# Kernel optimization log

Measured on AMD Instinct MI355X. Metric: run time of the kernel, lower is better.

## Reference

```python
import jax, jax.numpy as jnp
import numpy as np

SAMPLE_NUMS = 9
VIEW_RANGE = 2      # args.max_turn_view_range
TEMP = 0.07         # args.temperature
AVG_EPS = 1e-6      # BertAVG eps
COS_EPS = 1e-8      # torch.cosine_similarity eps


def setup_inputs() -> dict:
    key = jax.random.key(0)
    k0, k1, k2 = jax.random.split(key, 3)
    G, S, H = 8, 512, 768            # groups, max_seq_length, hidden_size
    B = G * SAMPLE_NUMS              # 72 flattened dialogues
    self_output = jax.random.normal(k0, (B, S, H), dtype=jnp.float32)
    attention_mask = jnp.ones((B, S), dtype=jnp.float32)
    qa_ids = jax.random.randint(k1, (B, S), 0, 4, dtype=jnp.int32)
    turn_ids = jnp.sort(jax.random.randint(k2, (B, S), 0, 16, dtype=jnp.int32), axis=-1)
    labels = jnp.zeros((G, SAMPLE_NUMS), dtype=jnp.float32).at[:, 0].set(1.0)
    return {"self_output": self_output, "attention_mask": attention_mask,
            "labels": labels, "qa_ids": qa_ids, "turn_ids": turn_ids}


def _masked_avg(x, m):
    # BertAVG: sum over seq of x*m / (sum(m) + eps)   x:[B,S,H] m:[B,S]
    return jnp.sum(x * m[..., None], axis=1) / (jnp.sum(m, axis=1, keepdims=True) + AVG_EPS)


def _cos(x, y):
    # torch.cosine_similarity over last dim, eps-clamped norms
    dot = jnp.sum(x * y, axis=-1)
    nx = jnp.maximum(jnp.linalg.norm(x, axis=-1), COS_EPS)
    ny = jnp.maximum(jnp.linalg.norm(y, axis=-1), COS_EPS)
    c = dot / (nx * ny)
    c = jnp.where(c == 1.0, jnp.nan, c)   # cos[cos==1] = nan
    return c / TEMP


def _calc_loss(pred, labels):
    return -jnp.nanmean(jax.nn.log_softmax(pred, axis=-1) * labels)


def reference(self_output, attention_mask, labels, qa_ids, turn_ids):
    H = self_output.shape[-1]
    # role masks from qa_ids
    q_mask = ((qa_ids == 1) | (qa_ids == 2)).astype(self_output.dtype)
    a_mask = ((qa_ids == 0) | (qa_ids == 2)).astype(self_output.dtype)
    n_mask = (qa_ids == 3).astype(self_output.dtype)
    q_am = attention_mask * q_mask
    a_am = attention_mask * a_mask
    n_am = attention_mask * n_mask
    q_so = self_output * q_am[..., None]   # [B,S,H]
    a_so = self_output * a_am[..., None]
    n_so = self_output * n_am[..., None]
    # role-masked cross scores [B,S,S]
    q_w = jnp.einsum('bsh,bth->bst', q_so, a_so + n_so)
    a_w = jnp.einsum('bsh,bth->bst', a_so, q_so + n_so)
    n_w = jnp.einsum('bsh,bth->bst', n_so, q_so + a_so)
    # turn-range band mask: |turn_s - turn_t| <= range
    dt = turn_ids[:, :, None] - turn_ids[:, None, :]
    band = (jnp.abs(dt) <= VIEW_RANGE).astype(self_output.dtype)  # [B,S,S]
    filtered_w = (q_w + a_w + n_w) * band
    # cross outputs
    q_co = jnp.einsum('bst,bth->bsh', filtered_w, q_so)
    a_co = jnp.einsum('bst,bth->bsh', filtered_w, a_so)
    n_co = jnp.einsum('bst,bth->bsh', filtered_w, n_so)
    # masked averages
    q_self = _masked_avg(q_so, q_am)
    q_cross = _masked_avg(q_co, a_am + n_am)
    a_self = _masked_avg(a_so, a_am)
    a_cross = _masked_avg(a_co, q_am + n_am)
    n_self = _masked_avg(n_so, n_am)
    n_cross = _masked_avg(n_co, q_am + a_am)
    # [G, sample_nums, H]
    q_self = q_self.reshape(-1, SAMPLE_NUMS, H)
    q_cross = q_cross.reshape(-1, SAMPLE_NUMS, H)
    a_self = a_self.reshape(-1, SAMPLE_NUMS, H)
    a_cross = a_cross.reshape(-1, SAMPLE_NUMS, H)
    n_self = n_self.reshape(-1, SAMPLE_NUMS, H)
    n_cross = n_cross.reshape(-1, SAMPLE_NUMS, H)
    q_output = q_self[:, 0, :]
    a_output = a_self[:, 0, :]
    n_output = n_self[:, 0, :]
    # vectorized over sample axis (replaces the python loop + stack)
    logit_q = _cos(q_self, q_cross)  # [G, sample_nums]
    logit_a = _cos(a_self, a_cross)
    logit_n = _cos(n_self, n_cross)
    stage_loss = (_calc_loss(logit_a, labels) + _calc_loss(logit_q, labels)
                  + _calc_loss(logit_n, labels)) / 3.0
    return (stage_loss, q_output, a_output, n_output)
```

## Files before the change

kernel.cpp:

```cpp
#include <hip/hip_runtime.h>
#include <math.h>

#define BB 72
#define SS 512
#define HH 768
#define GG 8
#define SN 9
#define VR 2
#define NT 16
#define NPART 16


__device__ float g_W[(size_t)BB * NT * 4 * HH];
__device__ float g_snum[BB * 3 * HH];
__device__ float g_xpart[(size_t)BB * NPART * 3 * HH];
__device__ float g_logits[3 * BB];

__device__ __forceinline__ void class_masks(float am, int id, float& qv, float& av, float& nv) {
    qv = (id == 1 || id == 2) ? am : 0.0f;
    av = (id == 0 || id == 2) ? am : 0.0f;
    nv = (id == 3) ? am : 0.0f;
}

__global__ void k_g(const float* __restrict__ x, const float* __restrict__ am,
                    const int* __restrict__ qa, const int* __restrict__ turn) {
    __shared__ float Gs[NT * 4 * 4 * 64];
    __shared__ int   tn[SS];
    __shared__ float c2[SS];
    __shared__ int   idv[SS];

    const int b = blockIdx.y, hbase = blockIdx.x * 256;
    const int tid = threadIdx.x, w = tid >> 6, lane = tid & 63;

    for (int i = tid; i < SS; i += 512) {
        tn[i] = turn[b * SS + i];
        float a = am[b * SS + i]; c2[i] = a * a;
        idv[i] = qa[b * SS + i];
    }
    {
        const float4 z = make_float4(0.f, 0.f, 0.f, 0.f);
        for (int i = tid * 4; i < NT * 4 * 4 * 64; i += 2048) *(float4*)&Gs[i] = z;
    }
    __syncthreads();

    const int s0 = w * 64;
    const float* xbase = x + ((size_t)b * SS + s0) * HH + hbase + lane * 4;
    float r[4][4];
#pragma unroll
    for (int i = 0; i < 4; ++i)
#pragma unroll
        for (int k = 0; k < 4; ++k) r[i][k] = 0.0f;
    int cur = tn[s0];

    float4 A[4], Bq[4];
#define LDQ(buf, c) { _Pragma("unroll") for (int j_ = 0; j_ < 4; ++j_)          \
        buf[j_] = *(const float4*)(xbase + (size_t)((c) * 4 + j_) * HH); }
#define FLUSH() { _Pragma("unroll") for (int i_ = 0; i_ < 4; ++i_) {            \
        _Pragma("unroll") for (int k_ = 0; k_ < 4; ++k_) {                      \
            atomicAdd(&Gs[((cur * 4 + i_) * 4 + k_) * 64 + lane], r[i_][k_]);   \
            r[i_][k_] = 0.0f; } } }
#define CONSUME(buf, c) { _Pragma("unroll") for (int j_ = 0; j_ < 4; ++j_) {    \
        const int s_ = s0 + (c) * 4 + j_;                                       \
        const int v_ = tn[s_];                                                  \
        if (v_ != cur) { FLUSH(); cur = v_; }                                   \
        const float c2_ = c2[s_];                                               \
        const int id_ = idv[s_];                                                \
        const float4 xv_ = buf[j_];                                             \
        if (id_ == 0) { r[0][0] += xv_.x * c2_; r[0][1] += xv_.y * c2_;         \
                        r[0][2] += xv_.z * c2_; r[0][3] += xv_.w * c2_; }       \
        else if (id_ == 1) { r[1][0] += xv_.x * c2_; r[1][1] += xv_.y * c2_;    \
                             r[1][2] += xv_.z * c2_; r[1][3] += xv_.w * c2_; }  \
        else if (id_ == 2) { r[2][0] += xv_.x * c2_; r[2][1] += xv_.y * c2_;    \
                             r[2][2] += xv_.z * c2_; r[2][3] += xv_.w * c2_; }  \
        else { r[3][0] += xv_.x * c2_; r[3][1] += xv_.y * c2_;                  \
               r[3][2] += xv_.z * c2_; r[3][3] += xv_.w * c2_; } } }

    LDQ(A, 0);
    for (int c = 0; c < 16; c += 2) {
        LDQ(Bq, c + 1);
        CONSUME(A, c);
        if (c + 2 < 16) LDQ(A, c + 2);
        CONSUME(Bq, c + 1);
    }
    FLUSH();
#undef LDQ
#undef FLUSH
#undef CONSUME
    __syncthreads();

#pragma unroll
    for (int vv = 0; vv < 2; ++vv) {
        const int v = w * 2 + vv;
        const int ulo = (v - VR < 0) ? 0 : v - VR;
        const int uhi = (v + VR > NT - 1) ? NT - 1 : v + VR;
        float acc[4][4];
#pragma unroll
        for (int i = 0; i < 4; ++i)
#pragma unroll
            for (int k = 0; k < 4; ++k) acc[i][k] = 0.0f;
        for (int u = ulo; u <= uhi; ++u) {
#pragma unroll
            for (int i = 0; i < 4; ++i)
#pragma unroll
                for (int k = 0; k < 4; ++k)
                    acc[i][k] += Gs[((u * 4 + i) * 4 + k) * 64 + lane];
        }
        float* Wo = g_W + ((size_t)(b * NT + v) * 4) * HH + hbase + lane * 4;
#pragma unroll
        for (int i = 0; i < 4; ++i) {
            float4 o; o.x = acc[i][0]; o.y = acc[i][1]; o.z = acc[i][2]; o.w = acc[i][3];
            *(float4*)(Wo + (size_t)i * HH) = o;
        }
    }
    if (w == 0) {
        float t[4][4];
#pragma unroll
        for (int i = 0; i < 4; ++i)
#pragma unroll
            for (int k = 0; k < 4; ++k) t[i][k] = 0.0f;
        for (int u = 0; u < NT; ++u) {
#pragma unroll
            for (int i = 0; i < 4; ++i)
#pragma unroll
                for (int k = 0; k < 4; ++k)
                    t[i][k] += Gs[((u * 4 + i) * 4 + k) * 64 + lane];
        }
        float4 oq, oa, on;
        oq.x = t[1][0] + t[2][0]; oq.y = t[1][1] + t[2][1];
        oq.z = t[1][2] + t[2][2]; oq.w = t[1][3] + t[2][3];
        oa.x = t[0][0] + t[2][0]; oa.y = t[0][1] + t[2][1];
        oa.z = t[0][2] + t[2][2]; oa.w = t[0][3] + t[2][3];
        on.x = t[3][0]; on.y = t[3][1]; on.z = t[3][2]; on.w = t[3][3];
        *(float4*)(g_snum + (size_t)(b * 3 + 0) * HH + hbase + lane * 4) = oq;
        *(float4*)(g_snum + (size_t)(b * 3 + 1) * HH + hbase + lane * 4) = oa;
        *(float4*)(g_snum + (size_t)(b * 3 + 2) * HH + hbase + lane * 4) = on;
    }
}

__global__ __launch_bounds__(256) void k_ct(const float* __restrict__ x,
                                            const float* __restrict__ am,
                                            const int* __restrict__ qa,
                                            const int* __restrict__ turn) {
    __shared__ float red[4][3 * HH];
    __shared__ int   tnb[32];
    __shared__ float amb[32];
    __shared__ int   idb[32];

    const int b = blockIdx.y, ts = blockIdx.x, T0 = ts * 32;
    const int tid = threadIdx.x, w = tid >> 6, lane = tid & 63;
    if (tid < 32) {
        tnb[tid] = turn[b * SS + T0 + tid];
        amb[tid] = am[b * SS + T0 + tid];
        idb[tid] = qa[b * SS + T0 + tid];
    }
    __syncthreads();

    const float* xb = x + (size_t)b * SS * HH;
    float4 xt[8][3];
#pragma unroll
    for (int it = 0; it < 8; ++it) {
        const float* xr = xb + (size_t)(T0 + w * 8 + it) * HH + lane * 4;
        xt[it][0] = *(const float4*)(xr + 0);
        xt[it][1] = *(const float4*)(xr + 256);
        xt[it][2] = *(const float4*)(xr + 512);
    }

    float xn[3][12];
#pragma unroll
    for (int c = 0; c < 3; ++c)
#pragma unroll
        for (int k = 0; k < 12; ++k) xn[c][k] = 0.0f;

    float4 Wr[4][3];
    int curv = -1;

#pragma unroll
    for (int it = 0; it < 8; ++it) {
        const int tl = w * 8 + it;
        const int v = tnb[tl];
        if (v != curv) {
            curv = v;
            const float* Wg = g_W + ((size_t)(b * NT + v) * 4) * HH + lane * 4;
#pragma unroll
            for (int i = 0; i < 4; ++i) {
                Wr[i][0] = *(const float4*)(Wg + (size_t)i * HH + 0);
                Wr[i][1] = *(const float4*)(Wg + (size_t)i * HH + 256);
                Wr[i][2] = *(const float4*)(Wg + (size_t)i * HH + 512);
            }
        }
        float d[4];
#pragma unroll
        for (int i = 0; i < 4; ++i) {
            float s = 0;
#pragma unroll
            for (int ch = 0; ch < 3; ++ch) {
                s += xt[it][ch].x * Wr[i][ch].x + xt[it][ch].y * Wr[i][ch].y
                   + xt[it][ch].z * Wr[i][ch].z + xt[it][ch].w * Wr[i][ch].w;
            }
            d[i] = s;
        }
#pragma unroll
        for (int off = 32; off; off >>= 1) {
#pragma unroll
            for (int i = 0; i < 4; ++i) d[i] += __shfl_xor(d[i], off);
        }
        float qt, at, nt; class_masks(amb[tl], idb[tl], qt, at, nt);
        const float ant = at + nt, qnt = qt + nt, qat = qt + at;
        const float Sqq = d[1] + d[2], Sqa = d[2], Saa = d[0] + d[2], Snn = d[3];
        const float cwq = qt * (ant * Sqa + qnt * Saa + qat * Snn);
        const float cwa = at * (ant * Sqq + qnt * Sqa + qat * Snn);
        const float cwn = nt * (ant * (Sqq + Sqa) + qnt * (Sqa + Saa));
#pragma unroll
        for (int ch = 0; ch < 3; ++ch) {
            const float4 xv = xt[it][ch];
            xn[0][ch * 4 + 0] += cwq * xv.x; xn[0][ch * 4 + 1] += cwq * xv.y;
            xn[0][ch * 4 + 2] += cwq * xv.z; xn[0][ch * 4 + 3] += cwq * xv.w;
            xn[1][ch * 4 + 0] += cwa * xv.x; xn[1][ch * 4 + 1] += cwa * xv.y;
            xn[1][ch * 4 + 2] += cwa * xv.z; xn[1][ch * 4 + 3] += cwa * xv.w;
            xn[2][ch * 4 + 0] += cwn * xv.x; xn[2][ch * 4 + 1] += cwn * xv.y;
            xn[2][ch * 4 + 2] += cwn * xv.z; xn[2][ch * 4 + 3] += cwn * xv.w;
        }
    }

#pragma unroll
    for (int c = 0; c < 3; ++c) {
#pragma unroll
        for (int ch = 0; ch < 3; ++ch) {
            float4 o;
            o.x = xn[c][ch * 4 + 0]; o.y = xn[c][ch * 4 + 1];
            o.z = xn[c][ch * 4 + 2]; o.w = xn[c][ch * 4 + 3];
            *(float4*)&red[w][c * HH + ch * 256 + lane * 4] = o;
        }
    }
    __syncthreads();
    float* xo = g_xpart + (size_t)(b * NPART + ts) * 3 * HH;
    for (int idx = tid * 4; idx < 3 * HH; idx += 1024) {
        float4 r0 = *(float4*)&red[0][idx];
        float4 r1 = *(float4*)&red[1][idx];
        float4 r2 = *(float4*)&red[2][idx];
        float4 r3 = *(float4*)&red[3][idx];
        float4 o;
        o.x = r0.x + r1.x + r2.x + r3.x;
        o.y = r0.y + r1.y + r2.y + r3.y;
        o.z = r0.z + r1.z + r2.z + r3.z;
        o.w = r0.w + r1.w + r2.w + r3.w;
        *(float4*)(xo + idx) = o;
    }
}

__global__ void k_cos(const float* __restrict__ am, const int* __restrict__ qa,
                      float* __restrict__ out) {
    const int c = blockIdx.x, b = blockIdx.y, tid = threadIdx.x;
    const int wave = tid >> 6, lane = tid & 63;
    __shared__ float redd[4][3];
    __shared__ float sD[3];

    float q = 0, a = 0, n = 0;
    for (int s = tid; s < SS; s += 256) {
        float m = am[b * SS + s]; int id = qa[b * SS + s];
        float qv, av, nv; class_masks(m, id, qv, av, nv);
        q += qv; a += av; n += nv;
    }
#pragma unroll
    for (int off = 32; off; off >>= 1) {
        q += __shfl_down(q, off); a += __shfl_down(a, off); n += __shfl_down(n, off);
    }
    if (lane == 0) { redd[wave][0] = q; redd[wave][1] = a; redd[wave][2] = n; }
    __syncthreads();
    if (tid == 0) {
        float Q = 0, A = 0, N = 0;
#pragma unroll
        for (int w = 0; w < 4; ++w) { Q += redd[w][0]; A += redd[w][1]; N += redd[w][2]; }
        sD[0] = Q; sD[1] = A; sD[2] = N;
    }
    __syncthreads();
    const float Dq = sD[0], Da = sD[1], Dn = sD[2];
    const float Dself = (c == 0) ? Dq : ((c == 1) ? Da : Dn);
    const float Dcross = (c == 0) ? (Da + Dn) : ((c == 1) ? (Dq + Dn) : (Dq + Da));
    const float invS = 1.0f / (Dself + 1e-6f), invC = 1.0f / (Dcross + 1e-6f);

    float dot = 0, n1 = 0, n2 = 0;
#pragma unroll
    for (int j = 0; j < 3; ++j) {
        const int h = tid + j * 256;
        float sv = g_snum[(size_t)(b * 3 + c) * HH + h];
        float cv = 0;
        const float* xp = g_xpart + ((size_t)b * NPART * 3 + c) * HH + h;
#pragma unroll
        for (int p = 0; p < NPART; ++p) cv += xp[(size_t)p * 3 * HH];
        sv *= invS; cv *= invC;
        dot += sv * cv; n1 += sv * sv; n2 += cv * cv;
        if (b % SN == 0)
            out[1 + ((size_t)c * GG + b / SN) * HH + h] = sv;
    }
#pragma unroll
    for (int off = 32; off; off >>= 1) {
        dot += __shfl_down(dot, off); n1 += __shfl_down(n1, off); n2 += __shfl_down(n2, off);
    }
    __shared__ float red2[4][3];
    if (lane == 0) { red2[wave][0] = dot; red2[wave][1] = n1; red2[wave][2] = n2; }
    __syncthreads();
    if (tid == 0) {
        float D = 0, N1 = 0, N2 = 0;
#pragma unroll
        for (int w = 0; w < 4; ++w) { D += red2[w][0]; N1 += red2[w][1]; N2 += red2[w][2]; }
        float nx = fmaxf(sqrtf(N1), 1e-8f);
        float ny = fmaxf(sqrtf(N2), 1e-8f);
        float cc = D / (nx * ny);
        if (cc == 1.0f) cc = __uint_as_float(0x7FC00000u);
        g_logits[c * BB + b] = cc / 0.07f;
    }
}

__global__ void k_loss(const float* __restrict__ labels, float* __restrict__ out) {
    __shared__ float rs[24];
    __shared__ int rc[24];
    const int tid = threadIdx.x;
    if (tid < 24) {
        int c = tid / GG, g = tid % GG;
        float lg[SN]; bool anynan = false;
        for (int j = 0; j < SN; ++j) {
            float v = g_logits[c * BB + g * SN + j];
            lg[j] = v;
            anynan = anynan || isnan(v);
        }
        float ssum = 0; int cnt = 0;
        if (!anynan) {
            float m = -1e30f;
            for (int j = 0; j < SN; ++j) m = fmaxf(m, lg[j]);
            float se = 0;
            for (int j = 0; j < SN; ++j) se += expf(lg[j] - m);
            float lse = m + logf(se);
            for (int j = 0; j < SN; ++j) ssum += (lg[j] - lse) * labels[g * SN + j];
            cnt = SN;
        }
        rs[tid] = ssum; rc[tid] = cnt;
    }
    __syncthreads();
    if (tid == 0) {
        float total = 0;
        for (int c = 0; c < 3; ++c) {
            float s = 0; int n = 0;
            for (int g = 0; g < GG; ++g) { s += rs[c * GG + g]; n += rc[c * GG + g]; }
            total += -(s / (float)n);
        }
        out[0] = total / 3.0f;
    }
}

extern "C" void kernel_launch(void* const* d_in, const int* in_sizes, int n_in,
                              void* d_out, int out_size, void* d_ws, size_t ws_size,
                              hipStream_t stream) {
    const float* x      = (const float*)d_in[0];
    const float* am     = (const float*)d_in[1];
    const float* labels = (const float*)d_in[2];
    const int*   qa     = (const int*)d_in[3];
    const int*   turn   = (const int*)d_in[4];
    float* out = (float*)d_out;

    k_g   <<<dim3(HH / 256, BB), 512, 0, stream>>>(x, am, qa, turn);
    k_ct  <<<dim3(SS / 32, BB),  256, 0, stream>>>(x, am, qa, turn);
    k_cos <<<dim3(3, BB),        256, 0, stream>>>(am, qa, out);
    k_loss<<<dim3(1),            64,  0, stream>>>(labels, out);
}
```

Baseline: 241.6 us.

## Split per-turn accumulation across sequence chunks with global atomics, defer window sums

The per-turn class accumulation kernel now runs over 8 sequence chunks per (batch, hidden slice), giving many more blocks. Partial results go to a zeroed global buffer through global atomics instead of shared-memory atomics. The view-range window sum moves into k_ct, and the full-sequence self sums move into k_cos, which now read the raw per-turn table. This trades extra global atomics, a zeroing kernel, and repeated window-sum reads for more parallelism in the first stage.

```diff
diff --git a/kernel.cpp b/kernel.cpp
--- a/kernel.cpp
+++ b/kernel.cpp
@@ -11,8 +11,7 @@
 #define NPART 16
 
 
-__device__ float g_W[(size_t)BB * NT * 4 * HH];
-__device__ float g_snum[BB * 3 * HH];
+__device__ float g_G[(size_t)BB * NT * 4 * HH];
 __device__ float g_xpart[(size_t)BB * NPART * 3 * HH];
 __device__ float g_logits[3 * BB];
 
@@ -22,119 +21,71 @@
     nv = (id == 3) ? am : 0.0f;
 }
 
-__global__ void k_g(const float* __restrict__ x, const float* __restrict__ am,
-                    const int* __restrict__ qa, const int* __restrict__ turn) {
-    __shared__ float Gs[NT * 4 * 4 * 64];
-    __shared__ int   tn[SS];
-    __shared__ float c2[SS];
-    __shared__ int   idv[SS];
-
-    const int b = blockIdx.y, hbase = blockIdx.x * 256;
+__global__ void k_zero() {
+    const size_t i = ((size_t)blockIdx.x * 256 + threadIdx.x) * 4;
+    *(float4*)&g_G[i] = make_float4(0.f, 0.f, 0.f, 0.f);
+}
+
+__global__ __launch_bounds__(256) void k_g(const float* __restrict__ x,
+                                           const float* __restrict__ am,
+                                           const int* __restrict__ qa,
+                                           const int* __restrict__ turn) {
+    __shared__ int   tn[64];
+    __shared__ float c2[64];
+    __shared__ int   idv[64];
+
+    const int b = blockIdx.y, hbase = blockIdx.x * 256, s0b = blockIdx.z * 64;
     const int tid = threadIdx.x, w = tid >> 6, lane = tid & 63;
 
-    for (int i = tid; i < SS; i += 512) {
-        tn[i] = turn[b * SS + i];
-        float a = am[b * SS + i]; c2[i] = a * a;
-        idv[i] = qa[b * SS + i];
-    }
-    {
-        const float4 z = make_float4(0.f, 0.f, 0.f, 0.f);
-        for (int i = tid * 4; i < NT * 4 * 4 * 64; i += 2048) *(float4*)&Gs[i] = z;
-    }
-    __syncthreads();
-
-    const int s0 = w * 64;
-    const float* xbase = x + ((size_t)b * SS + s0) * HH + hbase + lane * 4;
+    if (tid < 64) {
+        const int s = s0b + tid;
+        tn[tid] = turn[b * SS + s];
+        float a = am[b * SS + s]; c2[tid] = a * a;
+        idv[tid] = qa[b * SS + s];
+    }
+    __syncthreads();
+
+    const int sw = w * 16;
+    const float* xbase = x + ((size_t)(b * SS + s0b + sw)) * HH + hbase + lane * 4;
+
+    float4 xr[16];
+#pragma unroll
+    for (int j = 0; j < 16; ++j)
+        xr[j] = *(const float4*)(xbase + (size_t)j * HH);
+
     float r[4][4];
 #pragma unroll
     for (int i = 0; i < 4; ++i)
 #pragma unroll
         for (int k = 0; k < 4; ++k) r[i][k] = 0.0f;
-    int cur = tn[s0];
-
-    float4 A[4], Bq[4];
-#define LDQ(buf, c) { _Pragma("unroll") for (int j_ = 0; j_ < 4; ++j_)          \
-        buf[j_] = *(const float4*)(xbase + (size_t)((c) * 4 + j_) * HH); }
-#define FLUSH() { _Pragma("unroll") for (int i_ = 0; i_ < 4; ++i_) {            \
-        _Pragma("unroll") for (int k_ = 0; k_ < 4; ++k_) {                      \
-            atomicAdd(&Gs[((cur * 4 + i_) * 4 + k_) * 64 + lane], r[i_][k_]);   \
-            r[i_][k_] = 0.0f; } } }
-#define CONSUME(buf, c) { _Pragma("unroll") for (int j_ = 0; j_ < 4; ++j_) {    \
-        const int s_ = s0 + (c) * 4 + j_;                                       \
-        const int v_ = tn[s_];                                                  \
-        if (v_ != cur) { FLUSH(); cur = v_; }                                   \
-        const float c2_ = c2[s_];                                               \
-        const int id_ = idv[s_];                                                \
-        const float4 xv_ = buf[j_];                                             \
-        if (id_ == 0) { r[0][0] += xv_.x * c2_; r[0][1] += xv_.y * c2_;         \
-                        r[0][2] += xv_.z * c2_; r[0][3] += xv_.w * c2_; }       \
-        else if (id_ == 1) { r[1][0] += xv_.x * c2_; r[1][1] += xv_.y * c2_;    \
-                             r[1][2] += xv_.z * c2_; r[1][3] += xv_.w * c2_; }  \
-        else if (id_ == 2) { r[2][0] += xv_.x * c2_; r[2][1] += xv_.y * c2_;    \
-                             r[2][2] += xv_.z * c2_; r[2][3] += xv_.w * c2_; }  \
-        else { r[3][0] += xv_.x * c2_; r[3][1] += xv_.y * c2_;                  \
-               r[3][2] += xv_.z * c2_; r[3][3] += xv_.w * c2_; } } }
-
-    LDQ(A, 0);
-    for (int c = 0; c < 16; c += 2) {
-        LDQ(Bq, c + 1);
-        CONSUME(A, c);
-        if (c + 2 < 16) LDQ(A, c + 2);
-        CONSUME(Bq, c + 1);
+    int cur = tn[sw];
+
+#define FLUSH() {                                                              \
+    float* gb_ = g_G + ((size_t)(b * NT + cur) * 4) * HH + hbase + lane * 4;   \
+    _Pragma("unroll") for (int i_ = 0; i_ < 4; ++i_)                           \
+        _Pragma("unroll") for (int k_ = 0; k_ < 4; ++k_) {                     \
+            atomicAdd(gb_ + (size_t)i_ * HH + k_, r[i_][k_]);                  \
+            r[i_][k_] = 0.0f; } }
+
+#pragma unroll
+    for (int j = 0; j < 16; ++j) {
+        const int sl = sw + j;
+        const int v = tn[sl];
+        if (v != cur) { FLUSH(); cur = v; }
+        const float cc = c2[sl];
+        const int id = idv[sl];
+        const float4 xv = xr[j];
+        if (id == 0) { r[0][0] += xv.x * cc; r[0][1] += xv.y * cc;
+                       r[0][2] += xv.z * cc; r[0][3] += xv.w * cc; }
+        else if (id == 1) { r[1][0] += xv.x * cc; r[1][1] += xv.y * cc;
+                            r[1][2] += xv.z * cc; r[1][3] += xv.w * cc; }
+        else if (id == 2) { r[2][0] += xv.x * cc; r[2][1] += xv.y * cc;
+                            r[2][2] += xv.z * cc; r[2][3] += xv.w * cc; }
+        else { r[3][0] += xv.x * cc; r[3][1] += xv.y * cc;
+               r[3][2] += xv.z * cc; r[3][3] += xv.w * cc; }
     }
     FLUSH();
-#undef LDQ
 #undef FLUSH
-#undef CONSUME
-    __syncthreads();
-
-#pragma unroll
-    for (int vv = 0; vv < 2; ++vv) {
-        const int v = w * 2 + vv;
-        const int ulo = (v - VR < 0) ? 0 : v - VR;
-        const int uhi = (v + VR > NT - 1) ? NT - 1 : v + VR;
-        float acc[4][4];
-#pragma unroll
-        for (int i = 0; i < 4; ++i)
-#pragma unroll
-            for (int k = 0; k < 4; ++k) acc[i][k] = 0.0f;
-        for (int u = ulo; u <= uhi; ++u) {
-#pragma unroll
-            for (int i = 0; i < 4; ++i)
-#pragma unroll
-                for (int k = 0; k < 4; ++k)
-                    acc[i][k] += Gs[((u * 4 + i) * 4 + k) * 64 + lane];
-        }
-        float* Wo = g_W + ((size_t)(b * NT + v) * 4) * HH + hbase + lane * 4;
-#pragma unroll
-        for (int i = 0; i < 4; ++i) {
-            float4 o; o.x = acc[i][0]; o.y = acc[i][1]; o.z = acc[i][2]; o.w = acc[i][3];
-            *(float4*)(Wo + (size_t)i * HH) = o;
-        }
-    }
-    if (w == 0) {
-        float t[4][4];
-#pragma unroll
-        for (int i = 0; i < 4; ++i)
-#pragma unroll
-            for (int k = 0; k < 4; ++k) t[i][k] = 0.0f;
-        for (int u = 0; u < NT; ++u) {
-#pragma unroll
-            for (int i = 0; i < 4; ++i)
-#pragma unroll
-                for (int k = 0; k < 4; ++k)
-                    t[i][k] += Gs[((u * 4 + i) * 4 + k) * 64 + lane];
-        }
-        float4 oq, oa, on;
-        oq.x = t[1][0] + t[2][0]; oq.y = t[1][1] + t[2][1];
-        oq.z = t[1][2] + t[2][2]; oq.w = t[1][3] + t[2][3];
-        oa.x = t[0][0] + t[2][0]; oa.y = t[0][1] + t[2][1];
-        oa.z = t[0][2] + t[2][2]; oa.w = t[0][3] + t[2][3];
-        on.x = t[3][0]; on.y = t[3][1]; on.z = t[3][2]; on.w = t[3][3];
-        *(float4*)(g_snum + (size_t)(b * 3 + 0) * HH + hbase + lane * 4) = oq;
-        *(float4*)(g_snum + (size_t)(b * 3 + 1) * HH + hbase + lane * 4) = oa;
-        *(float4*)(g_snum + (size_t)(b * 3 + 2) * HH + hbase + lane * 4) = on;
-    }
 }
 
 __global__ __launch_bounds__(256) void k_ct(const float* __restrict__ x,
@@ -180,12 +131,24 @@
         const int v = tnb[tl];
         if (v != curv) {
             curv = v;
-            const float* Wg = g_W + ((size_t)(b * NT + v) * 4) * HH + lane * 4;
-#pragma unroll
-            for (int i = 0; i < 4; ++i) {
-                Wr[i][0] = *(const float4*)(Wg + (size_t)i * HH + 0);
-                Wr[i][1] = *(const float4*)(Wg + (size_t)i * HH + 256);
-                Wr[i][2] = *(const float4*)(Wg + (size_t)i * HH + 512);
+            const int ulo = (v - VR < 0) ? 0 : v - VR;
+            const int uhi = (v + VR > NT - 1) ? NT - 1 : v + VR;
+#pragma unroll
+            for (int i = 0; i < 4; ++i)
+#pragma unroll
+                for (int ch = 0; ch < 3; ++ch)
+                    Wr[i][ch] = make_float4(0.f, 0.f, 0.f, 0.f);
+            for (int u = ulo; u <= uhi; ++u) {
+                const float* Gg = g_G + ((size_t)(b * NT + u) * 4) * HH + lane * 4;
+#pragma unroll
+                for (int i = 0; i < 4; ++i) {
+#pragma unroll
+                    for (int ch = 0; ch < 3; ++ch) {
+                        const float4 gv = *(const float4*)(Gg + (size_t)i * HH + ch * 256);
+                        Wr[i][ch].x += gv.x; Wr[i][ch].y += gv.y;
+                        Wr[i][ch].z += gv.z; Wr[i][ch].w += gv.w;
+                    }
+                }
             }
         }
         float d[4];
@@ -283,7 +246,18 @@
 #pragma unroll
     for (int j = 0; j < 3; ++j) {
         const int h = tid + j * 256;
-        float sv = g_snum[(size_t)(b * 3 + c) * HH + h];
+        const float* Gb = g_G + ((size_t)b * NT * 4) * HH + h;
+        float sv = 0;
+        if (c == 0) {
+            for (int u = 0; u < NT; ++u)
+                sv += Gb[(size_t)(u * 4 + 1) * HH] + Gb[(size_t)(u * 4 + 2) * HH];
+        } else if (c == 1) {
+            for (int u = 0; u < NT; ++u)
+                sv += Gb[(size_t)(u * 4 + 0) * HH] + Gb[(size_t)(u * 4 + 2) * HH];
+        } else {
+            for (int u = 0; u < NT; ++u)
+                sv += Gb[(size_t)(u * 4 + 3) * HH];
+        }
         float cv = 0;
         const float* xp = g_xpart + ((size_t)b * NPART * 3 + c) * HH + h;
 #pragma unroll
@@ -358,8 +332,9 @@
     const int*   turn   = (const int*)d_in[4];
     float* out = (float*)d_out;
 
-    k_g   <<<dim3(HH / 256, BB), 512, 0, stream>>>(x, am, qa, turn);
-    k_ct  <<<dim3(SS / 32, BB),  256, 0, stream>>>(x, am, qa, turn);
-    k_cos <<<dim3(3, BB),        256, 0, stream>>>(am, qa, out);
-    k_loss<<<dim3(1),            64,  0, stream>>>(labels, out);
-}
+    k_zero<<<dim3(3456),            256, 0, stream>>>();
+    k_g   <<<dim3(HH / 256, BB, 8), 256, 0, stream>>>(x, am, qa, turn);
+    k_ct  <<<dim3(SS / 32, BB),     256, 0, stream>>>(x, am, qa, turn);
+    k_cos <<<dim3(3, BB),           256, 0, stream>>>(am, qa, out);
+    k_loss<<<dim3(1),               64,  0, stream>>>(labels, out);
+}
```

Result: slower. 388.5 us (+60.8%).
